# Performance work log

Measured on AMD Instinct MI355X. Metric: run time of the kernel, lower is better.

Reference implementation:

```python
import jax, jax.numpy as jnp
import numpy as np

B = 1
S = 256          # sequence_size (pair repr is S x S)
C = 128          # channel_size_pair
NHEAD = 4
HID = 32         # hidden_channel
SCALE = 1.0 / float(np.sqrt(HID))
EPS = 1e-5


def setup_inputs() -> dict:
    key = jax.random.key(0)
    ks = jax.random.split(key, 9)
    init = 0.02
    return {
        "pair_repr": jax.random.normal(ks[0], (B, S, S, C), dtype=jnp.float32),
        "gamma": jnp.ones((C,), dtype=jnp.float32),
        "beta": jnp.zeros((C,), dtype=jnp.float32),
        "Wq": jax.random.normal(ks[1], (C, NHEAD * HID), dtype=jnp.float32) * init,
        "Wk": jax.random.normal(ks[2], (C, NHEAD * HID), dtype=jnp.float32) * init,
        "Wv": jax.random.normal(ks[3], (C, NHEAD * HID), dtype=jnp.float32) * init,
        "Wb": jax.random.normal(ks[4], (C, NHEAD), dtype=jnp.float32) * init,
        "Wg": jax.random.normal(ks[5], (C, NHEAD * HID), dtype=jnp.float32) * init,
        "bg": jnp.zeros((NHEAD * HID,), dtype=jnp.float32),
        "Wo": jax.random.normal(ks[6], (NHEAD * HID, C), dtype=jnp.float32) * init,
        "bo": jnp.zeros((C,), dtype=jnp.float32),
    }


def _to_heads(t):
    # [b, h, w, n*d] -> [b, n, h, w, d]
    b, h, w, _ = t.shape
    return t.reshape(b, h, w, NHEAD, HID).transpose(0, 3, 1, 2, 4)


def reference(pair_repr, gamma, beta, Wq, Wk, Wv, Wb, Wg, bg, Wo, bo):
    # LayerNorm over channel dim
    mu = jnp.mean(pair_repr, axis=-1, keepdims=True)
    var = jnp.var(pair_repr, axis=-1, keepdims=True)
    z = (pair_repr - mu) * jax.lax.rsqrt(var + EPS) * gamma + beta

    q = _to_heads(z @ Wq)  # [b, n, i, j, d]
    k = _to_heads(z @ Wk)
    v = _to_heads(z @ Wv)
    g = _to_heads(jax.nn.sigmoid(z @ Wg + bg))

    # bias: [b, h, w, n] -> [b, n, h, w]; 'ending' broadcasts it over the j axis
    bias = (z @ Wb).transpose(0, 3, 1, 2)

    # 'ending' branch: attend over the row index k for each column j
    dots = SCALE * jnp.einsum('bnijd,bnkjd->bnijk', q, k) + bias[:, :, :, None, :]
    attn = jax.nn.softmax(dots, axis=4)
    out = g * jnp.einsum('bnijk,bnkjd->bnijd', attn, v)

    # [b, n, i, j, d] -> [b, i, j, n*d]
    out = out.transpose(0, 2, 3, 1, 4).reshape(B, S, S, NHEAD * HID)
    return out @ Wo + bo
```

## Files before the change

kernel.cpp:

```cpp
#include <hip/hip_runtime.h>
#include <hip/hip_bf16.h>
#include <math.h>

#define SCALE 0.1767766952966369f
#define LN_EPS 1e-5f

typedef short bf16x8 __attribute__((ext_vector_type(8)));
typedef float f32x4 __attribute__((ext_vector_type(4)));

__device__ __forceinline__ unsigned short f2bf(float f) {
    __hip_bfloat16 h = __float2bfloat16(f);
    return *reinterpret_cast<unsigned short*>(&h);
}
__device__ __forceinline__ float bf2f(unsigned short u) {
    union { unsigned int u32; float f; } c;
    c.u32 = ((unsigned int)u) << 16;
    return c.f;
}
__device__ __forceinline__ unsigned int pack2(float a, float b) {
    return (unsigned int)f2bf(a) | ((unsigned int)f2bf(b) << 16);
}

__global__ __launch_bounds__(256)
void k_prep(const float* __restrict__ Wq, const float* __restrict__ Wk,
            const float* __restrict__ Wv, const float* __restrict__ Wg,
            const float* __restrict__ Wo, const float* __restrict__ Wb,
            unsigned short* __restrict__ WT, unsigned short* __restrict__ WbT)
{
    if (blockIdx.x == 20) {
        int t = threadIdx.x;
        int row = t >> 4, k0 = (t & 15) * 8;
        unsigned int u[4];
        #pragma unroll
        for (int e = 0; e < 4; ++e) {
            float a = 0.f, b = 0.f;
            if (row < 4) {
                a = Wb[(k0 + 2*e    )*4 + row];
                b = Wb[(k0 + 2*e + 1)*4 + row];
            }
            u[e] = pack2(a, b);
        }
        *(uint4*)(WbT + row*128 + k0) = make_uint4(u[0], u[1], u[2], u[3]);
        return;
    }
    int idx = blockIdx.x * 256 + threadIdx.x;
    int m   = idx >> 10;
    int col = (idx >> 3) & 127;
    int k0  = (idx & 7) * 16;
    const float* W = (m==0) ? Wq : (m==1) ? Wk : (m==2) ? Wv : (m==3) ? Wg : Wo;
    unsigned int u[8];
    #pragma unroll
    for (int e = 0; e < 8; ++e) {
        float a = W[(k0 + 2*e    )*128 + col];
        float b = W[(k0 + 2*e + 1)*128 + col];
        u[e] = pack2(a, b);
    }
    uint4* dst = (uint4*)(WT + m*16384 + col*128 + k0);
    dst[0] = make_uint4(u[0], u[1], u[2], u[3]);
    dst[1] = make_uint4(u[4], u[5], u[6], u[7]);
}

__global__ __launch_bounds__(256)
void k_ln_proj(const float* __restrict__ x, const float* __restrict__ gamma,
               const float* __restrict__ beta,
               const unsigned short* __restrict__ WT,
               const unsigned short* __restrict__ WbT,
               const float* __restrict__ bg,
               unsigned short* __restrict__ Q, unsigned short* __restrict__ K,
               unsigned short* __restrict__ VT, unsigned short* __restrict__ G,
               float* __restrict__ BIAS)
{
    __shared__ unsigned short Wbuf[64*136];
    __shared__ unsigned short stg[4][2176];

    const int t    = threadIdx.x;
    const int lane = t & 63, w = t >> 6;
    const int l15  = lane & 15, quad = lane >> 4;
    const int j    = blockIdx.x >> 2;
    const int ti   = (blockIdx.x & 3) * 64 + w*16;
    unsigned short* sw = stg[w];

    float v[32];
    {
        const float* xr = x + ((size_t)(ti + l15)*256 + j)*128;
        float sum = 0.f, ssq = 0.f;
        #pragma unroll
        for (int kt = 0; kt < 4; ++kt) {
            float4 f0 = *(const float4*)(xr + kt*32 + quad*8);
            float4 f1 = *(const float4*)(xr + kt*32 + quad*8 + 4);
            v[kt*8+0]=f0.x; v[kt*8+1]=f0.y; v[kt*8+2]=f0.z; v[kt*8+3]=f0.w;
            v[kt*8+4]=f1.x; v[kt*8+5]=f1.y; v[kt*8+6]=f1.z; v[kt*8+7]=f1.w;
            sum += f0.x+f0.y+f0.z+f0.w + f1.x+f1.y+f1.z+f1.w;
            ssq += f0.x*f0.x+f0.y*f0.y+f0.z*f0.z+f0.w*f0.w
                 + f1.x*f1.x+f1.y*f1.y+f1.z*f1.z+f1.w*f1.w;
        }
        sum += __shfl_xor(sum, 16); ssq += __shfl_xor(ssq, 16);
        sum += __shfl_xor(sum, 32); ssq += __shfl_xor(ssq, 32);
        float mu  = sum * (1.f/128.f);
        float var = ssq * (1.f/128.f) - mu*mu;
        float rs  = rsqrtf(var + LN_EPS);
        #pragma unroll
        for (int kt = 0; kt < 4; ++kt)
            #pragma unroll
            for (int e = 0; e < 8; ++e) {
                int c = kt*32 + quad*8 + e;
                v[kt*8+e] = (v[kt*8+e]-mu)*rs*gamma[c] + beta[c];
            }
    }
    bf16x8 afrag[4];
    #pragma unroll
    for (int kt = 0; kt < 4; ++kt)
        #pragma unroll
        for (int e = 0; e < 8; ++e)
            afrag[kt][e] = (short)f2bf(v[kt*8+e]);

    {
        f32x4 bacc = (f32x4){0.f,0.f,0.f,0.f};
        #pragma unroll
        for (int kt = 0; kt < 4; ++kt) {
            bf16x8 b = *(const bf16x8*)(WbT + (size_t)l15*128 + kt*32 + quad*8);
            bacc = __builtin_amdgcn_mfma_f32_16x16x32_bf16(afrag[kt], b, bacc, 0, 0, 0);
        }
        if (l15 < 4) {
            #pragma unroll
            for (int reg = 0; reg < 4; ++reg)
                BIAS[l15*65536 + ((ti >> 2) + quad)*1024 + j*4 + reg] = bacc[reg];
        }
    }

    #pragma unroll 1
    for (int mm = 0; mm < 4; ++mm) {
        f32x4 acc[8];
        #pragma unroll
        for (int nt = 0; nt < 8; ++nt) acc[nt] = (f32x4){0.f,0.f,0.f,0.f};

        #pragma unroll 1
        for (int half = 0; half < 2; ++half) {
            __syncthreads();
            #pragma unroll
            for (int r = 0; r < 4; ++r) {
                int idx = r*256 + t;
                int col = idx >> 4, kc = idx & 15;
                *(uint4*)&Wbuf[col*136 + kc*8] =
                    *(const uint4*)&WT[mm*16384 + (half*64 + col)*128 + kc*8];
            }
            __syncthreads();

            #pragma unroll
            for (int kt = 0; kt < 4; ++kt) {
                #pragma unroll
                for (int nt2 = 0; nt2 < 4; ++nt2) {
                    bf16x8 b = *(const bf16x8*)&Wbuf[(nt2*16 + l15)*136 + kt*32 + quad*8];
                    if (mm == 2)
                        acc[half*4 + nt2] = __builtin_amdgcn_mfma_f32_16x16x32_bf16(
                            b, afrag[kt], acc[half*4 + nt2], 0, 0, 0);
                    else
                        acc[half*4 + nt2] = __builtin_amdgcn_mfma_f32_16x16x32_bf16(
                            afrag[kt], b, acc[half*4 + nt2], 0, 0, 0);
                }
            }
        }

        if (mm == 2) {
            #pragma unroll
            for (int nt = 0; nt < 8; ++nt)
                #pragma unroll
                for (int reg = 0; reg < 4; ++reg)
                    sw[(nt*16 + quad*4 + reg)*16 + l15] = f2bf(acc[nt][reg]);
            #pragma unroll
            for (int it = 0; it < 4; ++it) {
                int idx = it*64 + lane;
                int ch = idx >> 1, c = idx & 1;
                uint4 val = *(const uint4*)&sw[ch*16 + c*8];
                int nh = ch >> 5, d = ch & 31;
                *(uint4*)&VT[(((size_t)(nh*256 + j))*32 + d)*256 + ti + c*8] = val;
            }
        } else {
            #pragma unroll
            for (int nt = 0; nt < 8; ++nt) {
                int cc = nt*16 + l15;
                float bgv = (mm == 3) ? bg[cc] : 0.f;
                #pragma unroll
                for (int reg = 0; reg < 4; ++reg) {
                    float val = acc[nt][reg];
                    if (mm == 0)      val *= SCALE;
                    else if (mm == 3) val = 1.f/(1.f + __expf(-(val + bgv)));
                    sw[(quad*4 + reg)*136 + cc] = f2bf(val);
                }
            }
            {
                int row = lane >> 2, c = lane & 3;
                unsigned short* Dst = (mm == 0) ? Q : (mm == 1) ? K : G;
                #pragma unroll
                for (int nh = 0; nh < 4; ++nh) {
                    uint4 val = *(const uint4*)&sw[row*136 + nh*32 + c*8];
                    *(uint4*)&Dst[(((size_t)(nh*256 + j))*256 + ti + row)*32 + c*8] = val;
                }
            }
        }
    }
}

__global__ __launch_bounds__(256)
void k_attn(const unsigned short* __restrict__ Q, const unsigned short* __restrict__ K,
            const unsigned short* __restrict__ VT, const unsigned short* __restrict__ G,
            const float* __restrict__ BIAS, unsigned short* __restrict__ AO)
{
    __shared__ unsigned short P_lds[4][16*264];

    const int t    = threadIdx.x;
    const int n    = blockIdx.x >> 10;
    const int j    = (blockIdx.x >> 2) & 255;
    const int ic   = blockIdx.x & 3;
    const int lane = t & 63, w = t >> 6;
    const int l15  = lane & 15, quad = lane >> 4;
    const int i0   = ic*64 + w*16;

    const size_t nb = (size_t)(n*256 + j);
    const unsigned short* qb  = Q  + nb*8192;
    const unsigned short* kb  = K  + nb*8192;
    const unsigned short* vtb = VT + nb*8192;
    const unsigned short* gb  = G  + nb*8192;
    const float* biasn = BIAS + n*65536;
    unsigned short* Pw = P_lds[w];

    bf16x8 a = *(const bf16x8*)(qb + (size_t)(i0 + l15)*32 + quad*8);
    f32x4 acc[16];
    #pragma unroll
    for (int kt = 0; kt < 16; ++kt) {
        bf16x8 b = *(const bf16x8*)(kb + (size_t)(kt*16 + l15)*32 + quad*8);
        acc[kt] = __builtin_amdgcn_mfma_f32_16x16x32_bf16(a, b, (f32x4){0.f,0.f,0.f,0.f}, 0, 0, 0);
    }

    float mx[4] = {-1e30f, -1e30f, -1e30f, -1e30f};
    #pragma unroll
    for (int kt = 0; kt < 16; ++kt) {
        float4 bv = *(const float4*)&biasn[((i0 >> 2) + quad)*1024 + (kt*16 + l15)*4];
        acc[kt][0] += bv.x; acc[kt][1] += bv.y;
        acc[kt][2] += bv.z; acc[kt][3] += bv.w;
        #pragma unroll
        for (int reg = 0; reg < 4; ++reg)
            mx[reg] = fmaxf(mx[reg], acc[kt][reg]);
    }
    #pragma unroll
    for (int m = 1; m <= 8; m <<= 1) {
        #pragma unroll
        for (int reg = 0; reg < 4; ++reg)
            mx[reg] = fmaxf(mx[reg], __shfl_xor(mx[reg], m));
    }

    float sm[4] = {0.f, 0.f, 0.f, 0.f};
    #pragma unroll
    for (int kt = 0; kt < 16; ++kt) {
        #pragma unroll
        for (int reg = 0; reg < 4; ++reg) {
            float e = __expf(acc[kt][reg] - mx[reg]);
            acc[kt][reg] = e;
            sm[reg] += e;
        }
    }
    #pragma unroll
    for (int m = 1; m <= 8; m <<= 1) {
        #pragma unroll
        for (int reg = 0; reg < 4; ++reg)
            sm[reg] += __shfl_xor(sm[reg], m);
    }
    float rinv[4];
    #pragma unroll
    for (int reg = 0; reg < 4; ++reg) rinv[reg] = 1.f / sm[reg];

    #pragma unroll
    for (int kt = 0; kt < 16; ++kt) {
        #pragma unroll
        for (int reg = 0; reg < 4; ++reg)
            Pw[(quad*4 + reg)*264 + kt*16 + l15] = f2bf(acc[kt][reg]);
    }

    f32x4 o[2];
    o[0] = (f32x4){0.f,0.f,0.f,0.f};
    o[1] = (f32x4){0.f,0.f,0.f,0.f};
    #pragma unroll
    for (int kt8 = 0; kt8 < 8; ++kt8) {
        bf16x8 pa = *(const bf16x8*)(Pw + l15*264 + kt8*32 + quad*8);
        #pragma unroll
        for (int nt = 0; nt < 2; ++nt) {
            bf16x8 vb = *(const bf16x8*)(vtb + (size_t)(nt*16 + l15)*256 + kt8*32 + quad*8);
            o[nt] = __builtin_amdgcn_mfma_f32_16x16x32_bf16(pa, vb, o[nt], 0, 0, 0);
        }
    }

    #pragma unroll
    for (int nt = 0; nt < 2; ++nt) {
        #pragma unroll
        for (int reg = 0; reg < 4; ++reg) {
            int i = i0 + quad*4 + reg;
            float g = bf2f(gb[(size_t)i*32 + nt*16 + l15]);
            float res = o[nt][reg] * rinv[reg] * g;
            Pw[(quad*4 + reg)*40 + nt*16 + l15] = f2bf(res);
        }
    }
    {
        int row = lane >> 2, oo = lane & 3;
        uint4 val = *(const uint4*)&Pw[row*40 + oo*8];
        *(uint4*)&AO[((size_t)((i0 + row)*256 + j))*128 + n*32 + oo*8] = val;
    }
}

__global__ __launch_bounds__(64)
void k_out(const unsigned short* __restrict__ AO, const unsigned short* __restrict__ WOT,
           const float* __restrict__ bo, float* __restrict__ out)
{
    const int t    = threadIdx.x;
    const int l15  = t & 15, quad = t >> 4;
    const int p0   = (blockIdx.x >> 1) * 16;
    const int cb   = (blockIdx.x & 1) * 64;

    bf16x8 a[4];
    #pragma unroll
    for (int kt = 0; kt < 4; ++kt)
        a[kt] = *(const bf16x8*)(AO + (size_t)(p0 + l15)*128 + kt*32 + quad*8);

    f32x4 acc[4];
    #pragma unroll
    for (int nt = 0; nt < 4; ++nt) acc[nt] = (f32x4){0.f,0.f,0.f,0.f};
    #pragma unroll
    for (int kt = 0; kt < 4; ++kt) {
        #pragma unroll
        for (int nt = 0; nt < 4; ++nt) {
            bf16x8 b = *(const bf16x8*)(WOT + (size_t)(cb + nt*16 + l15)*128 + kt*32 + quad*8);
            acc[nt] = __builtin_amdgcn_mfma_f32_16x16x32_bf16(a[kt], b, acc[nt], 0, 0, 0);
        }
    }
    #pragma unroll
    for (int nt = 0; nt < 4; ++nt) {
        float bov = bo[cb + nt*16 + l15];
        #pragma unroll
        for (int reg = 0; reg < 4; ++reg) {
            int p = p0 + quad*4 + reg;
            out[(size_t)p*128 + cb + nt*16 + l15] = acc[nt][reg] + bov;
        }
    }
}

extern "C" void kernel_launch(void* const* d_in, const int* in_sizes, int n_in,
                              void* d_out, int out_size, void* d_ws, size_t ws_size,
                              hipStream_t stream) {
    (void)in_sizes; (void)n_in; (void)out_size; (void)ws_size;
    const float* x     = (const float*)d_in[0];
    const float* gamma = (const float*)d_in[1];
    const float* beta  = (const float*)d_in[2];
    const float* Wq    = (const float*)d_in[3];
    const float* Wk    = (const float*)d_in[4];
    const float* Wv    = (const float*)d_in[5];
    const float* Wb    = (const float*)d_in[6];
    const float* Wg    = (const float*)d_in[7];
    const float* bg    = (const float*)d_in[8];
    const float* Wo    = (const float*)d_in[9];
    const float* bo    = (const float*)d_in[10];
    float* out = (float*)d_out;

    unsigned short* WT  = (unsigned short*)d_ws;
    unsigned short* WbT = WT + 5*16384;
    unsigned short* Qp  = WbT + 2048;
    unsigned short* Kp  = Qp + 8388608;
    unsigned short* VTp = Kp + 8388608;
    unsigned short* Gp  = VTp + 8388608;
    float* Bp   = (float*)(Gp + 8388608);
    unsigned short* AOp = (unsigned short*)(Bp + 262144);
    unsigned short* WOT = WT + 4*16384;

    k_prep<<<21, 256, 0, stream>>>(Wq, Wk, Wv, Wg, Wo, Wb, WT, WbT);
    k_ln_proj<<<1024, 256, 0, stream>>>(x, gamma, beta, WT, WbT, bg,
                                        Qp, Kp, VTp, Gp, Bp);
    k_attn<<<4096, 256, 0, stream>>>(Qp, Kp, VTp, Gp, Bp, AOp);
    k_out<<<8192, 64, 0, stream>>>(AOp, WOT, bo, out);
}
```

Before: 224.5 us.

## Transpose QK^T MFMA and pass softmax probabilities via lane shuffles instead of LDS

Swaps the MFMA operands so each lane holds one query row's scores, which turns the softmax max and sum reductions into two cross-quad shuffles instead of sixteen. The bias tensor layout is changed to match, so bias loads stay contiguous float4s. The probability tile is now packed to bf16 in registers and rearranged into the PV MFMA A-operand layout with xor shuffles, removing the 16x264 LDS staging buffer and its round trip. The cost is extra shuffle and select instructions and more live registers.

New measurement: 242.5 us. 1.08x slower.

```diff
diff --git a/kernel.cpp b/kernel.cpp
--- a/kernel.cpp
+++ b/kernel.cpp
@@ -124,7 +124,7 @@
         if (l15 < 4) {
             #pragma unroll
             for (int reg = 0; reg < 4; ++reg)
-                BIAS[l15*65536 + ((ti >> 2) + quad)*1024 + j*4 + reg] = bacc[reg];
+                BIAS[l15*65536 + (ti + quad*4 + reg)*256 + j] = bacc[reg];
         }
     }
 
@@ -206,7 +206,7 @@
             const unsigned short* __restrict__ VT, const unsigned short* __restrict__ G,
             const float* __restrict__ BIAS, unsigned short* __restrict__ AO)
 {
-    __shared__ unsigned short P_lds[4][16*264];
+    __shared__ unsigned short stg[4][16*40];
 
     const int t    = threadIdx.x;
     const int n    = blockIdx.x >> 10;
@@ -222,66 +222,66 @@
     const unsigned short* vtb = VT + nb*8192;
     const unsigned short* gb  = G  + nb*8192;
     const float* biasn = BIAS + n*65536;
-    unsigned short* Pw = P_lds[w];
-
-    bf16x8 a = *(const bf16x8*)(qb + (size_t)(i0 + l15)*32 + quad*8);
+    unsigned short* sw = stg[w];
+
+    bf16x8 aq = *(const bf16x8*)(qb + (size_t)(i0 + l15)*32 + quad*8);
     f32x4 acc[16];
     #pragma unroll
     for (int kt = 0; kt < 16; ++kt) {
-        bf16x8 b = *(const bf16x8*)(kb + (size_t)(kt*16 + l15)*32 + quad*8);
-        acc[kt] = __builtin_amdgcn_mfma_f32_16x16x32_bf16(a, b, (f32x4){0.f,0.f,0.f,0.f}, 0, 0, 0);
-    }
-
-    float mx[4] = {-1e30f, -1e30f, -1e30f, -1e30f};
+        bf16x8 bk = *(const bf16x8*)(kb + (size_t)(kt*16 + l15)*32 + quad*8);
+        acc[kt] = __builtin_amdgcn_mfma_f32_16x16x32_bf16(bk, aq, (f32x4){0.f,0.f,0.f,0.f}, 0, 0, 0);
+    }
+
+    float mx = -1e30f;
     #pragma unroll
     for (int kt = 0; kt < 16; ++kt) {
-        float4 bv = *(const float4*)&biasn[((i0 >> 2) + quad)*1024 + (kt*16 + l15)*4];
+        float4 bv = *(const float4*)&biasn[(size_t)(i0 + l15)*256 + kt*16 + quad*4];
         acc[kt][0] += bv.x; acc[kt][1] += bv.y;
         acc[kt][2] += bv.z; acc[kt][3] += bv.w;
-        #pragma unroll
-        for (int reg = 0; reg < 4; ++reg)
-            mx[reg] = fmaxf(mx[reg], acc[kt][reg]);
-    }
-    #pragma unroll
-    for (int m = 1; m <= 8; m <<= 1) {
-        #pragma unroll
-        for (int reg = 0; reg < 4; ++reg)
-            mx[reg] = fmaxf(mx[reg], __shfl_xor(mx[reg], m));
-    }
-
-    float sm[4] = {0.f, 0.f, 0.f, 0.f};
+        mx = fmaxf(mx, fmaxf(fmaxf(acc[kt][0], acc[kt][1]),
+                             fmaxf(acc[kt][2], acc[kt][3])));
+    }
+    mx = fmaxf(mx, __shfl_xor(mx, 16));
+    mx = fmaxf(mx, __shfl_xor(mx, 32));
+
+    float sm = 0.f;
+    unsigned int pw0[16], pw1[16];
     #pragma unroll
     for (int kt = 0; kt < 16; ++kt) {
-        #pragma unroll
-        for (int reg = 0; reg < 4; ++reg) {
-            float e = __expf(acc[kt][reg] - mx[reg]);
-            acc[kt][reg] = e;
-            sm[reg] += e;
-        }
-    }
-    #pragma unroll
-    for (int m = 1; m <= 8; m <<= 1) {
-        #pragma unroll
-        for (int reg = 0; reg < 4; ++reg)
-            sm[reg] += __shfl_xor(sm[reg], m);
-    }
-    float rinv[4];
-    #pragma unroll
-    for (int reg = 0; reg < 4; ++reg) rinv[reg] = 1.f / sm[reg];
-
-    #pragma unroll
-    for (int kt = 0; kt < 16; ++kt) {
-        #pragma unroll
-        for (int reg = 0; reg < 4; ++reg)
-            Pw[(quad*4 + reg)*264 + kt*16 + l15] = f2bf(acc[kt][reg]);
-    }
-
+        float e0 = __expf(acc[kt][0] - mx);
+        float e1 = __expf(acc[kt][1] - mx);
+        float e2 = __expf(acc[kt][2] - mx);
+        float e3 = __expf(acc[kt][3] - mx);
+        sm += (e0 + e1) + (e2 + e3);
+        pw0[kt] = pack2(e0, e1);
+        pw1[kt] = pack2(e2, e3);
+    }
+    sm += __shfl_xor(sm, 16);
+    sm += __shfl_xor(sm, 32);
+    float rinv = 1.f / sm;
+
+    const bool h0 = (lane < 32);
     f32x4 o[2];
     o[0] = (f32x4){0.f,0.f,0.f,0.f};
     o[1] = (f32x4){0.f,0.f,0.f,0.f};
     #pragma unroll
     for (int kt8 = 0; kt8 < 8; ++kt8) {
-        bf16x8 pa = *(const bf16x8*)(Pw + l15*264 + kt8*32 + quad*8);
+        unsigned int E0 = pw0[2*kt8],     E1 = pw1[2*kt8];
+        unsigned int O0 = pw0[2*kt8 + 1], O1 = pw1[2*kt8 + 1];
+        unsigned int X0 = __shfl_xor(h0 ? O0 : E0, 32);
+        unsigned int X1 = __shfl_xor(h0 ? O1 : E1, 32);
+        unsigned int Y0 = __shfl_xor(X0, 16);
+        unsigned int Y1 = __shfl_xor(X1, 16);
+        unsigned int Z0 = __shfl_xor(h0 ? E0 : O0, 16);
+        unsigned int Z1 = __shfl_xor(h0 ? E1 : O1, 16);
+        unsigned int c0, c1, c2, c3;
+        if (quad == 0)      { c0 = E0; c1 = E1; c2 = Z0; c3 = Z1; }
+        else if (quad == 1) { c0 = Y0; c1 = Y1; c2 = X0; c3 = X1; }
+        else if (quad == 2) { c0 = X0; c1 = X1; c2 = Y0; c3 = Y1; }
+        else                { c0 = Z0; c1 = Z1; c2 = O0; c3 = O1; }
+        union { unsigned int u[4]; bf16x8 v; } pu;
+        pu.u[0] = c0; pu.u[1] = c1; pu.u[2] = c2; pu.u[3] = c3;
+        bf16x8 pa = pu.v;
         #pragma unroll
         for (int nt = 0; nt < 2; ++nt) {
             bf16x8 vb = *(const bf16x8*)(vtb + (size_t)(nt*16 + l15)*256 + kt8*32 + quad*8);
@@ -289,19 +289,24 @@
         }
     }
 
+    float r4[4];
+    #pragma unroll
+    for (int reg = 0; reg < 4; ++reg)
+        r4[reg] = __shfl(rinv, quad*4 + reg, 16);
+
     #pragma unroll
     for (int nt = 0; nt < 2; ++nt) {
         #pragma unroll
         for (int reg = 0; reg < 4; ++reg) {
             int i = i0 + quad*4 + reg;
             float g = bf2f(gb[(size_t)i*32 + nt*16 + l15]);
-            float res = o[nt][reg] * rinv[reg] * g;
-            Pw[(quad*4 + reg)*40 + nt*16 + l15] = f2bf(res);
+            float res = o[nt][reg] * r4[reg] * g;
+            sw[(quad*4 + reg)*40 + nt*16 + l15] = f2bf(res);
         }
     }
     {
         int row = lane >> 2, oo = lane & 3;
-        uint4 val = *(const uint4*)&Pw[row*40 + oo*8];
+        uint4 val = *(const uint4*)&sw[row*40 + oo*8];
         *(uint4*)&AO[((size_t)((i0 + row)*256 + j))*128 + n*32 + oo*8] = val;
     }
 }
```

## Transpose gate layout, fold log2e into softmax, stage Wo in LDS for output GEMM

Applied to the files above, without the earlier changes.

The gate tensor is now stored transposed (channel-major, like V) so the attention kernel can load it with vectorized loads early, instead of doing scattered per-element loads at the end. Q scale and bias are premultiplied by log2(e) so the softmax can use exp2f directly. The output projection now runs 256-thread blocks that stage all of Wo in LDS once and compute all 128 output columns per wave, which cuts redundant global weight reads. The cost is extra LDS and a block-wide sync in the output kernel.

After: 228.0 us. No clear change (+1.6%).

```diff
diff --git a/kernel.cpp b/kernel.cpp
--- a/kernel.cpp
+++ b/kernel.cpp
@@ -3,6 +3,8 @@
 #include <math.h>
 
 #define SCALE 0.1767766952966369f
+#define LOG2E 1.4426950408889634f
+#define QSCALE 0.25503487f
 #define LN_EPS 1e-5f
 
 typedef short bf16x8 __attribute__((ext_vector_type(8)));
@@ -67,7 +69,7 @@
                const unsigned short* __restrict__ WbT,
                const float* __restrict__ bg,
                unsigned short* __restrict__ Q, unsigned short* __restrict__ K,
-               unsigned short* __restrict__ VT, unsigned short* __restrict__ G,
+               unsigned short* __restrict__ VT, unsigned short* __restrict__ GT,
                float* __restrict__ BIAS)
 {
     __shared__ unsigned short Wbuf[64*136];
@@ -124,7 +126,7 @@
         if (l15 < 4) {
             #pragma unroll
             for (int reg = 0; reg < 4; ++reg)
-                BIAS[l15*65536 + ((ti >> 2) + quad)*1024 + j*4 + reg] = bacc[reg];
+                BIAS[l15*65536 + ((ti >> 2) + quad)*1024 + j*4 + reg] = bacc[reg] * LOG2E;
         }
     }
 
@@ -175,22 +177,39 @@
                 int nh = ch >> 5, d = ch & 31;
                 *(uint4*)&VT[(((size_t)(nh*256 + j))*32 + d)*256 + ti + c*8] = val;
             }
-        } else {
+        } else if (mm == 3) {
             #pragma unroll
             for (int nt = 0; nt < 8; ++nt) {
                 int cc = nt*16 + l15;
-                float bgv = (mm == 3) ? bg[cc] : 0.f;
+                float bgv = bg[cc];
+                float v0 = 1.f/(1.f + __expf(-(acc[nt][0] + bgv)));
+                float v1 = 1.f/(1.f + __expf(-(acc[nt][1] + bgv)));
+                float v2 = 1.f/(1.f + __expf(-(acc[nt][2] + bgv)));
+                float v3 = 1.f/(1.f + __expf(-(acc[nt][3] + bgv)));
+                *(uint2*)&sw[cc*16 + quad*4] = make_uint2(pack2(v0, v1), pack2(v2, v3));
+            }
+            #pragma unroll
+            for (int it = 0; it < 4; ++it) {
+                int idx = it*64 + lane;
+                int ch = idx >> 1, c = idx & 1;
+                uint4 val = *(const uint4*)&sw[ch*16 + c*8];
+                int nh = ch >> 5, d = ch & 31;
+                *(uint4*)&GT[(((size_t)(nh*256 + j))*32 + d)*256 + ti + c*8] = val;
+            }
+        } else {
+            #pragma unroll
+            for (int nt = 0; nt < 8; ++nt) {
+                int cc = nt*16 + l15;
                 #pragma unroll
                 for (int reg = 0; reg < 4; ++reg) {
                     float val = acc[nt][reg];
-                    if (mm == 0)      val *= SCALE;
-                    else if (mm == 3) val = 1.f/(1.f + __expf(-(val + bgv)));
+                    if (mm == 0) val *= QSCALE;
                     sw[(quad*4 + reg)*136 + cc] = f2bf(val);
                 }
             }
             {
                 int row = lane >> 2, c = lane & 3;
-                unsigned short* Dst = (mm == 0) ? Q : (mm == 1) ? K : G;
+                unsigned short* Dst = (mm == 0) ? Q : K;
                 #pragma unroll
                 for (int nh = 0; nh < 4; ++nh) {
                     uint4 val = *(const uint4*)&sw[row*136 + nh*32 + c*8];
@@ -203,7 +222,7 @@
 
 __global__ __launch_bounds__(256)
 void k_attn(const unsigned short* __restrict__ Q, const unsigned short* __restrict__ K,
-            const unsigned short* __restrict__ VT, const unsigned short* __restrict__ G,
+            const unsigned short* __restrict__ VT, const unsigned short* __restrict__ GT,
             const float* __restrict__ BIAS, unsigned short* __restrict__ AO)
 {
     __shared__ unsigned short P_lds[4][16*264];
@@ -220,9 +239,12 @@
     const unsigned short* qb  = Q  + nb*8192;
     const unsigned short* kb  = K  + nb*8192;
     const unsigned short* vtb = VT + nb*8192;
-    const unsigned short* gb  = G  + nb*8192;
+    const unsigned short* gtb = GT + nb*8192;
     const float* biasn = BIAS + n*65536;
     unsigned short* Pw = P_lds[w];
+
+    uint2 gw0 = *(const uint2*)(gtb + (size_t)l15*256        + i0 + quad*4);
+    uint2 gw1 = *(const uint2*)(gtb + (size_t)(16 + l15)*256 + i0 + quad*4);
 
     bf16x8 a = *(const bf16x8*)(qb + (size_t)(i0 + l15)*32 + quad*8);
     f32x4 acc[16];
@@ -254,7 +276,7 @@
     for (int kt = 0; kt < 16; ++kt) {
         #pragma unroll
         for (int reg = 0; reg < 4; ++reg) {
-            float e = __expf(acc[kt][reg] - mx[reg]);
+            float e = exp2f(acc[kt][reg] - mx[reg]);
             acc[kt][reg] = e;
             sm[reg] += e;
         }
@@ -289,13 +311,16 @@
         }
     }
 
+    float gg[2][4] = {
+        { bf2f((unsigned short)(gw0.x & 0xffff)), bf2f((unsigned short)(gw0.x >> 16)),
+          bf2f((unsigned short)(gw0.y & 0xffff)), bf2f((unsigned short)(gw0.y >> 16)) },
+        { bf2f((unsigned short)(gw1.x & 0xffff)), bf2f((unsigned short)(gw1.x >> 16)),
+          bf2f((unsigned short)(gw1.y & 0xffff)), bf2f((unsigned short)(gw1.y >> 16)) } };
     #pragma unroll
     for (int nt = 0; nt < 2; ++nt) {
         #pragma unroll
         for (int reg = 0; reg < 4; ++reg) {
-            int i = i0 + quad*4 + reg;
-            float g = bf2f(gb[(size_t)i*32 + nt*16 + l15]);
-            float res = o[nt][reg] * rinv[reg] * g;
+            float res = o[nt][reg] * rinv[reg] * gg[nt][reg];
             Pw[(quad*4 + reg)*40 + nt*16 + l15] = f2bf(res);
         }
     }
@@ -306,38 +331,49 @@
     }
 }
 
-__global__ __launch_bounds__(64)
+__global__ __launch_bounds__(256)
 void k_out(const unsigned short* __restrict__ AO, const unsigned short* __restrict__ WOT,
            const float* __restrict__ bo, float* __restrict__ out)
 {
+    __shared__ unsigned short WB[128*136];
+
     const int t    = threadIdx.x;
-    const int l15  = t & 15, quad = t >> 4;
-    const int p0   = (blockIdx.x >> 1) * 16;
-    const int cb   = (blockIdx.x & 1) * 64;
+    const int lane = t & 63, w = t >> 6;
+    const int l15  = lane & 15, quad = lane >> 4;
+    const int p0   = (blockIdx.x*4 + w) * 16;
+
+    #pragma unroll
+    for (int r = 0; r < 8; ++r) {
+        int idx = r*256 + t;
+        int col = idx >> 4, kc = idx & 15;
+        *(uint4*)&WB[col*136 + kc*8] = *(const uint4*)&WOT[col*128 + kc*8];
+    }
 
     bf16x8 a[4];
     #pragma unroll
     for (int kt = 0; kt < 4; ++kt)
         a[kt] = *(const bf16x8*)(AO + (size_t)(p0 + l15)*128 + kt*32 + quad*8);
 
-    f32x4 acc[4];
-    #pragma unroll
-    for (int nt = 0; nt < 4; ++nt) acc[nt] = (f32x4){0.f,0.f,0.f,0.f};
+    __syncthreads();
+
+    f32x4 acc[8];
+    #pragma unroll
+    for (int nt = 0; nt < 8; ++nt) acc[nt] = (f32x4){0.f,0.f,0.f,0.f};
     #pragma unroll
     for (int kt = 0; kt < 4; ++kt) {
         #pragma unroll
-        for (int nt = 0; nt < 4; ++nt) {
-            bf16x8 b = *(const bf16x8*)(WOT + (size_t)(cb + nt*16 + l15)*128 + kt*32 + quad*8);
+        for (int nt = 0; nt < 8; ++nt) {
+            bf16x8 b = *(const bf16x8*)&WB[(nt*16 + l15)*136 + kt*32 + quad*8];
             acc[nt] = __builtin_amdgcn_mfma_f32_16x16x32_bf16(a[kt], b, acc[nt], 0, 0, 0);
         }
     }
     #pragma unroll
-    for (int nt = 0; nt < 4; ++nt) {
-        float bov = bo[cb + nt*16 + l15];
+    for (int nt = 0; nt < 8; ++nt) {
+        float bov = bo[nt*16 + l15];
         #pragma unroll
         for (int reg = 0; reg < 4; ++reg) {
             int p = p0 + quad*4 + reg;
-            out[(size_t)p*128 + cb + nt*16 + l15] = acc[nt][reg] + bov;
+            out[(size_t)p*128 + nt*16 + l15] = acc[nt][reg] + bov;
         }
     }
 }
@@ -364,14 +400,14 @@
     unsigned short* Qp  = WbT + 2048;
     unsigned short* Kp  = Qp + 8388608;
     unsigned short* VTp = Kp + 8388608;
-    unsigned short* Gp  = VTp + 8388608;
-    float* Bp   = (float*)(Gp + 8388608);
+    unsigned short* GTp = VTp + 8388608;
+    float* Bp   = (float*)(GTp + 8388608);
     unsigned short* AOp = (unsigned short*)(Bp + 262144);
     unsigned short* WOT = WT + 4*16384;
 
     k_prep<<<21, 256, 0, stream>>>(Wq, Wk, Wv, Wg, Wo, Wb, WT, WbT);
     k_ln_proj<<<1024, 256, 0, stream>>>(x, gamma, beta, WT, WbT, bg,
-                                        Qp, Kp, VTp, Gp, Bp);
-    k_attn<<<4096, 256, 0, stream>>>(Qp, Kp, VTp, Gp, Bp, AOp);
-    k_out<<<8192, 64, 0, stream>>>(AOp, WOT, bo, out);
-}
+                                        Qp, Kp, VTp, GTp, Bp);
+    k_attn<<<4096, 256, 0, stream>>>(Qp, Kp, VTp, GTp, Bp, AOp);
+    k_out<<<1024, 256, 0, stream>>>(AOp, WOT, bo, out);
+}
```

## Fuse output projection into attention kernel and loop heads per block

Applied to the files above, without the earlier changes.

Merges the attention and output-projection kernels. Each block now loops over all four heads for one column j, then immediately runs the Wo projection on the freshly written attention output rows. This removes one kernel launch and the separate full pass over the AO buffer. In exchange, the grid has fewer blocks with serial head iterations, and the AO round trip still goes through global memory.

Result: slower. 235.0 us (+4.7%).

```diff
diff --git a/kernel.cpp b/kernel.cpp
--- a/kernel.cpp
+++ b/kernel.cpp
@@ -202,142 +202,135 @@
 }
 
 __global__ __launch_bounds__(256)
-void k_attn(const unsigned short* __restrict__ Q, const unsigned short* __restrict__ K,
-            const unsigned short* __restrict__ VT, const unsigned short* __restrict__ G,
-            const float* __restrict__ BIAS, unsigned short* __restrict__ AO)
+void k_attn_out(const unsigned short* __restrict__ Q, const unsigned short* __restrict__ K,
+                const unsigned short* __restrict__ VT, const unsigned short* __restrict__ G,
+                const float* __restrict__ BIAS, unsigned short* __restrict__ AO,
+                const unsigned short* __restrict__ WOT, const float* __restrict__ bo,
+                float* __restrict__ out)
 {
     __shared__ unsigned short P_lds[4][16*264];
 
     const int t    = threadIdx.x;
-    const int n    = blockIdx.x >> 10;
-    const int j    = (blockIdx.x >> 2) & 255;
+    const int j    = blockIdx.x >> 2;
     const int ic   = blockIdx.x & 3;
     const int lane = t & 63, w = t >> 6;
     const int l15  = lane & 15, quad = lane >> 4;
     const int i0   = ic*64 + w*16;
-
-    const size_t nb = (size_t)(n*256 + j);
-    const unsigned short* qb  = Q  + nb*8192;
-    const unsigned short* kb  = K  + nb*8192;
-    const unsigned short* vtb = VT + nb*8192;
-    const unsigned short* gb  = G  + nb*8192;
-    const float* biasn = BIAS + n*65536;
     unsigned short* Pw = P_lds[w];
 
-    bf16x8 a = *(const bf16x8*)(qb + (size_t)(i0 + l15)*32 + quad*8);
-    f32x4 acc[16];
-    #pragma unroll
-    for (int kt = 0; kt < 16; ++kt) {
-        bf16x8 b = *(const bf16x8*)(kb + (size_t)(kt*16 + l15)*32 + quad*8);
-        acc[kt] = __builtin_amdgcn_mfma_f32_16x16x32_bf16(a, b, (f32x4){0.f,0.f,0.f,0.f}, 0, 0, 0);
-    }
-
-    float mx[4] = {-1e30f, -1e30f, -1e30f, -1e30f};
-    #pragma unroll
-    for (int kt = 0; kt < 16; ++kt) {
-        float4 bv = *(const float4*)&biasn[((i0 >> 2) + quad)*1024 + (kt*16 + l15)*4];
-        acc[kt][0] += bv.x; acc[kt][1] += bv.y;
-        acc[kt][2] += bv.z; acc[kt][3] += bv.w;
-        #pragma unroll
-        for (int reg = 0; reg < 4; ++reg)
-            mx[reg] = fmaxf(mx[reg], acc[kt][reg]);
-    }
-    #pragma unroll
-    for (int m = 1; m <= 8; m <<= 1) {
-        #pragma unroll
-        for (int reg = 0; reg < 4; ++reg)
-            mx[reg] = fmaxf(mx[reg], __shfl_xor(mx[reg], m));
-    }
-
-    float sm[4] = {0.f, 0.f, 0.f, 0.f};
-    #pragma unroll
-    for (int kt = 0; kt < 16; ++kt) {
+    #pragma unroll 1
+    for (int n = 0; n < 4; ++n) {
+        const size_t nb = (size_t)(n*256 + j);
+        const unsigned short* qb  = Q  + nb*8192;
+        const unsigned short* kb  = K  + nb*8192;
+        const unsigned short* vtb = VT + nb*8192;
+        const unsigned short* gb  = G  + nb*8192;
+        const float* biasn = BIAS + n*65536;
+
+        bf16x8 a = *(const bf16x8*)(qb + (size_t)(i0 + l15)*32 + quad*8);
+        f32x4 acc[16];
+        #pragma unroll
+        for (int kt = 0; kt < 16; ++kt) {
+            bf16x8 b = *(const bf16x8*)(kb + (size_t)(kt*16 + l15)*32 + quad*8);
+            acc[kt] = __builtin_amdgcn_mfma_f32_16x16x32_bf16(a, b, (f32x4){0.f,0.f,0.f,0.f}, 0, 0, 0);
+        }
+
+        float mx[4] = {-1e30f, -1e30f, -1e30f, -1e30f};
+        #pragma unroll
+        for (int kt = 0; kt < 16; ++kt) {
+            float4 bv = *(const float4*)&biasn[((i0 >> 2) + quad)*1024 + (kt*16 + l15)*4];
+            acc[kt][0] += bv.x; acc[kt][1] += bv.y;
+            acc[kt][2] += bv.z; acc[kt][3] += bv.w;
+            #pragma unroll
+            for (int reg = 0; reg < 4; ++reg)
+                mx[reg] = fmaxf(mx[reg], acc[kt][reg]);
+        }
+        #pragma unroll
+        for (int m = 1; m <= 8; m <<= 1) {
+            #pragma unroll
+            for (int reg = 0; reg < 4; ++reg)
+                mx[reg] = fmaxf(mx[reg], __shfl_xor(mx[reg], m));
+        }
+
+        float sm[4] = {0.f, 0.f, 0.f, 0.f};
+        #pragma unroll
+        for (int kt = 0; kt < 16; ++kt) {
+            #pragma unroll
+            for (int reg = 0; reg < 4; ++reg) {
+                float e = __expf(acc[kt][reg] - mx[reg]);
+                acc[kt][reg] = e;
+                sm[reg] += e;
+            }
+        }
+        #pragma unroll
+        for (int m = 1; m <= 8; m <<= 1) {
+            #pragma unroll
+            for (int reg = 0; reg < 4; ++reg)
+                sm[reg] += __shfl_xor(sm[reg], m);
+        }
+        float rinv[4];
+        #pragma unroll
+        for (int reg = 0; reg < 4; ++reg) rinv[reg] = 1.f / sm[reg];
+
+        #pragma unroll
+        for (int kt = 0; kt < 16; ++kt) {
+            #pragma unroll
+            for (int reg = 0; reg < 4; ++reg)
+                Pw[(quad*4 + reg)*264 + kt*16 + l15] = f2bf(acc[kt][reg]);
+        }
+
+        f32x4 o[2];
+        o[0] = (f32x4){0.f,0.f,0.f,0.f};
+        o[1] = (f32x4){0.f,0.f,0.f,0.f};
+        #pragma unroll
+        for (int kt8 = 0; kt8 < 8; ++kt8) {
+            bf16x8 pa = *(const bf16x8*)(Pw + l15*264 + kt8*32 + quad*8);
+            #pragma unroll
+            for (int nt = 0; nt < 2; ++nt) {
+                bf16x8 vb = *(const bf16x8*)(vtb + (size_t)(nt*16 + l15)*256 + kt8*32 + quad*8);
+                o[nt] = __builtin_amdgcn_mfma_f32_16x16x32_bf16(pa, vb, o[nt], 0, 0, 0);
+            }
+        }
+
+        #pragma unroll
+        for (int nt = 0; nt < 2; ++nt) {
+            #pragma unroll
+            for (int reg = 0; reg < 4; ++reg) {
+                int i = i0 + quad*4 + reg;
+                float g = bf2f(gb[(size_t)i*32 + nt*16 + l15]);
+                float res = o[nt][reg] * rinv[reg] * g;
+                Pw[(quad*4 + reg)*40 + nt*16 + l15] = f2bf(res);
+            }
+        }
+        {
+            int row = lane >> 2, oo = lane & 3;
+            uint4 val = *(const uint4*)&Pw[row*40 + oo*8];
+            *(uint4*)&AO[((size_t)((i0 + row)*256 + j))*128 + n*32 + oo*8] = val;
+        }
+    }
+
+    bf16x8 a2[4];
+    #pragma unroll
+    for (int kt = 0; kt < 4; ++kt)
+        a2[kt] = *(const bf16x8*)(AO + ((size_t)((i0 + l15)*256 + j))*128 + kt*32 + quad*8);
+
+    f32x4 acc2[8];
+    #pragma unroll
+    for (int nt = 0; nt < 8; ++nt) acc2[nt] = (f32x4){0.f,0.f,0.f,0.f};
+    #pragma unroll
+    for (int kt = 0; kt < 4; ++kt) {
+        #pragma unroll
+        for (int nt = 0; nt < 8; ++nt) {
+            bf16x8 b = *(const bf16x8*)(WOT + (size_t)(nt*16 + l15)*128 + kt*32 + quad*8);
+            acc2[nt] = __builtin_amdgcn_mfma_f32_16x16x32_bf16(a2[kt], b, acc2[nt], 0, 0, 0);
+        }
+    }
+    #pragma unroll
+    for (int nt = 0; nt < 8; ++nt) {
+        float bov = bo[nt*16 + l15];
         #pragma unroll
         for (int reg = 0; reg < 4; ++reg) {
-            float e = __expf(acc[kt][reg] - mx[reg]);
-            acc[kt][reg] = e;
-            sm[reg] += e;
-        }
-    }
-    #pragma unroll
-    for (int m = 1; m <= 8; m <<= 1) {
-        #pragma unroll
-        for (int reg = 0; reg < 4; ++reg)
-            sm[reg] += __shfl_xor(sm[reg], m);
-    }
-    float rinv[4];
-    #pragma unroll
-    for (int reg = 0; reg < 4; ++reg) rinv[reg] = 1.f / sm[reg];
-
-    #pragma unroll
-    for (int kt = 0; kt < 16; ++kt) {
-        #pragma unroll
-        for (int reg = 0; reg < 4; ++reg)
-            Pw[(quad*4 + reg)*264 + kt*16 + l15] = f2bf(acc[kt][reg]);
-    }
-
-    f32x4 o[2];
-    o[0] = (f32x4){0.f,0.f,0.f,0.f};
-    o[1] = (f32x4){0.f,0.f,0.f,0.f};
-    #pragma unroll
-    for (int kt8 = 0; kt8 < 8; ++kt8) {
-        bf16x8 pa = *(const bf16x8*)(Pw + l15*264 + kt8*32 + quad*8);
-        #pragma unroll
-        for (int nt = 0; nt < 2; ++nt) {
-            bf16x8 vb = *(const bf16x8*)(vtb + (size_t)(nt*16 + l15)*256 + kt8*32 + quad*8);
-            o[nt] = __builtin_amdgcn_mfma_f32_16x16x32_bf16(pa, vb, o[nt], 0, 0, 0);
-        }
-    }
-
-    #pragma unroll
-    for (int nt = 0; nt < 2; ++nt) {
-        #pragma unroll
-        for (int reg = 0; reg < 4; ++reg) {
-            int i = i0 + quad*4 + reg;
-            float g = bf2f(gb[(size_t)i*32 + nt*16 + l15]);
-            float res = o[nt][reg] * rinv[reg] * g;
-            Pw[(quad*4 + reg)*40 + nt*16 + l15] = f2bf(res);
-        }
-    }
-    {
-        int row = lane >> 2, oo = lane & 3;
-        uint4 val = *(const uint4*)&Pw[row*40 + oo*8];
-        *(uint4*)&AO[((size_t)((i0 + row)*256 + j))*128 + n*32 + oo*8] = val;
-    }
-}
-
-__global__ __launch_bounds__(64)
-void k_out(const unsigned short* __restrict__ AO, const unsigned short* __restrict__ WOT,
-           const float* __restrict__ bo, float* __restrict__ out)
-{
-    const int t    = threadIdx.x;
-    const int l15  = t & 15, quad = t >> 4;
-    const int p0   = (blockIdx.x >> 1) * 16;
-    const int cb   = (blockIdx.x & 1) * 64;
-
-    bf16x8 a[4];
-    #pragma unroll
-    for (int kt = 0; kt < 4; ++kt)
-        a[kt] = *(const bf16x8*)(AO + (size_t)(p0 + l15)*128 + kt*32 + quad*8);
-
-    f32x4 acc[4];
-    #pragma unroll
-    for (int nt = 0; nt < 4; ++nt) acc[nt] = (f32x4){0.f,0.f,0.f,0.f};
-    #pragma unroll
-    for (int kt = 0; kt < 4; ++kt) {
-        #pragma unroll
-        for (int nt = 0; nt < 4; ++nt) {
-            bf16x8 b = *(const bf16x8*)(WOT + (size_t)(cb + nt*16 + l15)*128 + kt*32 + quad*8);
-            acc[nt] = __builtin_amdgcn_mfma_f32_16x16x32_bf16(a[kt], b, acc[nt], 0, 0, 0);
-        }
-    }
-    #pragma unroll
-    for (int nt = 0; nt < 4; ++nt) {
-        float bov = bo[cb + nt*16 + l15];
-        #pragma unroll
-        for (int reg = 0; reg < 4; ++reg) {
-            int p = p0 + quad*4 + reg;
-            out[(size_t)p*128 + cb + nt*16 + l15] = acc[nt][reg] + bov;
+            out[((size_t)((i0 + quad*4 + reg)*256 + j))*128 + nt*16 + l15] = acc2[nt][reg] + bov;
         }
     }
 }
@@ -372,6 +365,5 @@
     k_prep<<<21, 256, 0, stream>>>(Wq, Wk, Wv, Wg, Wo, Wb, WT, WbT);
     k_ln_proj<<<1024, 256, 0, stream>>>(x, gamma, beta, WT, WbT, bg,
                                         Qp, Kp, VTp, Gp, Bp);
-    k_attn<<<4096, 256, 0, stream>>>(Qp, Kp, VTp, Gp, Bp, AOp);
-    k_out<<<8192, 64, 0, stream>>>(AOp, WOT, bo, out);
-}
+    k_attn_out<<<1024, 256, 0, stream>>>(Qp, Kp, VTp, Gp, Bp, AOp, WOT, bo, out);
+}
```
